# Kernel optimization log

Hardware: AMD Instinct MI355X
Metric: run time of the kernel (lower is better)

The kernel has to match this reference:

```python
import jax, jax.numpy as jnp
from jax import lax
import numpy as np


def setup_inputs() -> dict:
    key = jax.random.key(0)
    kx, kw = jax.random.split(key)
    # Binary {0,1} activations: the module's int8-cast/XOR/AND trick is only
    # meaningful XNOR-popcount math for binary inputs.
    x = jax.random.randint(kx, (32, 256, 58, 58), 0, 2).astype(jnp.float32)
    weight = jax.random.normal(kw, (256, 256, 3, 3), dtype=jnp.float32)
    return {"x": x, "weight": weight}


def reference(x, weight):
    # XNORConv2d.forward, stride=1, padding=0 (forward never pads).
    B, C, H, W = x.shape
    O, _, kh, kw = weight.shape
    n = C * H * W  # note: alpha normalizes by INPUT size, as in the source
    N = kh * kw

    # alpha = sum_{c,kh,kw} |w| / n, one scalar per output filter  -> (O,)
    alpha = jnp.sum(jnp.abs(weight), axis=(1, 2, 3)) / n

    # Binarized weights: sign(w) >= 0 -> {0,1}
    bw = (weight >= 0).astype(x.dtype)

    dn = lax.conv_dimension_numbers(x.shape, weight.shape, ("NCHW", "OIHW", "NCHW"))
    conv = lambda a, f: lax.conv_general_dilated(
        a, f, window_strides=(1, 1), padding="VALID", dimension_numbers=dn
    )

    # XNOR match count per (b, o, y, x): S = #(p==f) over c,kh,kw
    #   = conv(p, f) + conv(1-p, 1-f)
    S = conv(x, bw) + conv(1.0 - x, 1.0 - bw)  # (B, O, H', W')

    # popcount per channel = 2*s_c - N; summed over channels -> 2*S - C*N
    res = 2.0 * S - jnp.asarray(C * N, dtype=x.dtype)

    return alpha[None, :, None, None] * res
```

## Files before the change

kernel.cpp:

```cpp
#include <hip/hip_runtime.h>
#include <stdint.h>


#define BATCH 32
#define C_IN 256
#define OCH 256
#define HIN 58
#define WIN2 58
#define HOUT 56
#define WOUT 56
#define TAPS 9
#define WWORDS 8
#define HWIN (HIN * WIN2)
#define HWOUT (HOUT * WOUT)
#define NPOS (BATCH * HWIN)
#define OGRP 32

__global__ __launch_bounds__(256) void pack_x_kernel(
    const float* __restrict__ x, uint32_t* __restrict__ xp)
{
    int t = blockIdx.x * 256 + threadIdx.x;
    int w = t / (NPOS / 2);
    int q = t - w * (NPOS / 2);
    int p = 2 * q;
    int b = p / HWIN;
    int r = p - b * HWIN;
    const float* xb = x + ((size_t)(b * C_IN + w * 32)) * HWIN + r;
    uint32_t m0 = 0u, m1 = 0u;
    #pragma unroll
    for (int j = 0; j < 32; ++j) {
        float2 v = *(const float2*)(xb + (size_t)j * HWIN);
        m0 |= (v.x > 0.5f ? 1u : 0u) << j;
        m1 |= (v.y > 0.5f ? 1u : 0u) << j;
    }
    xp[(size_t)p * WWORDS + w] = m0;
    xp[(size_t)(p + 1) * WWORDS + w] = m1;
}

__global__ __launch_bounds__(256) void pack_w_kernel(
    const float* __restrict__ wt, uint32_t* __restrict__ wq,
    float* __restrict__ sA, float* __restrict__ sB)
{
    int o = blockIdx.x;
    int c = threadIdx.x;
    const float* wb = wt + ((size_t)o * C_IN + c) * TAPS;
    float wv[TAPS];
    float s = 0.f;
    #pragma unroll
    for (int t = 0; t < TAPS; ++t) {
        wv[t] = wb[t];
        s += fabsf(wv[t]);
    }
    int wave = c >> 6, lane = c & 63;
    #pragma unroll
    for (int t = 0; t < TAPS; ++t) {
        unsigned long long m = __ballot(wv[t] >= 0.0f);
        if (lane == 0) {
            wq[((size_t)t * OCH + o) * WWORDS + wave * 2]     = (uint32_t)m;
            wq[((size_t)t * OCH + o) * WWORDS + wave * 2 + 1] = (uint32_t)(m >> 32);
        }
    }
    __shared__ float red[256];
    red[c] = s;
    __syncthreads();
    for (int off = 128; off > 0; off >>= 1) {
        if (c < off) red[c] += red[c + off];
        __syncthreads();
    }
    if (c == 0) {
        float alpha = red[0] / (float)(C_IN * HWIN);
        sA[o] = -2.0f * alpha;
        sB[o] = (float)(C_IN * TAPS) * alpha;
    }
}

__global__ __launch_bounds__(256, 4) void xnor_main_kernel(
    const uint32_t* __restrict__ xp, const uint32_t* __restrict__ wq,
    const float* __restrict__ sA, const float* __restrict__ sB,
    float* __restrict__ out)
{
    __shared__ uint32_t wlds[TAPS * OGRP * WWORDS];

    int obase = blockIdx.y * OGRP;
    #pragma unroll
    for (int i = 0; i < 9; ++i) {
        int L = threadIdx.x + i * 256;
        int tap = L >> 8;
        int oo  = (L >> 3) & (OGRP - 1);
        int k   = L & 7;
        wlds[L] = wq[(((size_t)tap * OCH) + obase + oo) * WWORDS + k];
    }
    __syncthreads();

    int m = blockIdx.x * 256 + threadIdx.x;
    int b = m / HWOUT;
    int r = m - b * HWOUT;
    int oy = r / WOUT;
    int ox = r - oy * WOUT;

    uint32_t acc[OGRP / 2];
    #pragma unroll
    for (int i = 0; i < OGRP / 2; ++i) acc[i] = 0u;

    #pragma unroll 1
    for (int tap = 0; tap < TAPS; ++tap) {
        int dy = tap / 3, dx = tap - dy * 3;
        const uint4* src = (const uint4*)(xp +
            (((size_t)b * HIN + (oy + dy)) * WIN2 + (ox + dx)) * WWORDS);
        uint4 x0 = src[0];
        uint4 x1 = src[1];
        const uint4* wl = (const uint4*)&wlds[tap * OGRP * WWORDS];
        #pragma unroll
        for (int oo = 0; oo < OGRP; oo += 2) {
            uint4 wa = wl[oo * 2 + 0];
            uint4 wb2 = wl[oo * 2 + 1];
            uint4 wc = wl[oo * 2 + 2];
            uint4 wd = wl[oo * 2 + 3];
            uint32_t q0 = __popc(wa.x ^ x0.x) + __popc(wa.y ^ x0.y)
                        + __popc(wa.z ^ x0.z) + __popc(wa.w ^ x0.w);
            uint32_t q1 = __popc(wb2.x ^ x1.x) + __popc(wb2.y ^ x1.y)
                        + __popc(wb2.z ^ x1.z) + __popc(wb2.w ^ x1.w);
            uint32_t q2 = __popc(wc.x ^ x0.x) + __popc(wc.y ^ x0.y)
                        + __popc(wc.z ^ x0.z) + __popc(wc.w ^ x0.w);
            uint32_t q3 = __popc(wd.x ^ x1.x) + __popc(wd.y ^ x1.y)
                        + __popc(wd.z ^ x1.z) + __popc(wd.w ^ x1.w);
            acc[oo >> 1] += (q0 + q1) + ((q2 + q3) << 16);
        }
    }

    size_t ob = ((size_t)b * OCH + obase) * HWOUT + (size_t)oy * WOUT + ox;
    #pragma unroll
    for (int oo = 0; oo < OGRP; oo += 2) {
        uint32_t a = acc[oo >> 1];
        float P0 = (float)(a & 0xFFFFu);
        float P1 = (float)(a >> 16);
        int o0 = obase + oo;
        out[ob + (size_t)oo * HWOUT]       = fmaf(sA[o0],     P0, sB[o0]);
        out[ob + (size_t)(oo + 1) * HWOUT] = fmaf(sA[o0 + 1], P1, sB[o0 + 1]);
    }
}

extern "C" void kernel_launch(void* const* d_in, const int* in_sizes, int n_in,
                              void* d_out, int out_size, void* d_ws, size_t ws_size,
                              hipStream_t stream)
{
    const float* x  = (const float*)d_in[0];
    const float* wt = (const float*)d_in[1];
    float* out = (float*)d_out;

    char* ws = (char*)d_ws;
    uint32_t* xp = (uint32_t*)ws;
    uint32_t* wq = (uint32_t*)(ws + 3444736);
    float*    sA = (float*)(ws + 3444736 + 73728);
    float*    sB = (float*)(ws + 3444736 + 73728 + 1024);

    pack_x_kernel<<<dim3(1682), dim3(256), 0, stream>>>(x, xp);

    pack_w_kernel<<<dim3(OCH), dim3(256), 0, stream>>>(wt, wq, sA, sB);

    xnor_main_kernel<<<dim3(392, 8), dim3(256), 0, stream>>>(xp, wq, sA, sB, out);
}
```

Measured before the change: 316.8 us.

## Prefetch next tap's packed input, restructure packing writes, raise occupancy target

The main XNOR kernel now loads the next tap's packed activation words while computing the current tap, which hides global load latency behind popcount work. It also raises the launch-bounds occupancy hint from 4 to 8 blocks per CU, which limits registers per thread. The popcount accumulation is reordered so popcounts feed the accumulator directly, a form that may map onto the bitcount-accumulate instruction. The x packing kernel now has each thread handle one position and two 32-channel words, writing one 8-byte store instead of two strided 4-byte stores. In exchange the packing reads become scalar and less coalesced per lane, and the higher occupancy target risks register spilling.

```diff
diff --git a/kernel.cpp b/kernel.cpp
--- a/kernel.cpp
+++ b/kernel.cpp
@@ -20,21 +20,20 @@
     const float* __restrict__ x, uint32_t* __restrict__ xp)
 {
     int t = blockIdx.x * 256 + threadIdx.x;
-    int w = t / (NPOS / 2);
-    int q = t - w * (NPOS / 2);
-    int p = 2 * q;
+    int p  = t >> 2;
+    int wp = t & 3;
     int b = p / HWIN;
     int r = p - b * HWIN;
-    const float* xb = x + ((size_t)(b * C_IN + w * 32)) * HWIN + r;
+    const float* xb = x + ((size_t)(b * C_IN + wp * 64)) * HWIN + r;
     uint32_t m0 = 0u, m1 = 0u;
     #pragma unroll
     for (int j = 0; j < 32; ++j) {
-        float2 v = *(const float2*)(xb + (size_t)j * HWIN);
-        m0 |= (v.x > 0.5f ? 1u : 0u) << j;
-        m1 |= (v.y > 0.5f ? 1u : 0u) << j;
+        float v0 = xb[(size_t)j * HWIN];
+        float v1 = xb[(size_t)(j + 32) * HWIN];
+        m0 |= (v0 > 0.5f ? 1u : 0u) << j;
+        m1 |= (v1 > 0.5f ? 1u : 0u) << j;
     }
-    xp[(size_t)p * WWORDS + w] = m0;
-    xp[(size_t)(p + 1) * WWORDS + w] = m1;
+    *(uint2*)(xp + (size_t)p * WWORDS + wp * 2) = make_uint2(m0, m1);
 }
 
 __global__ __launch_bounds__(256) void pack_w_kernel(
@@ -74,12 +73,12 @@
     }
 }
 
-__global__ __launch_bounds__(256, 4) void xnor_main_kernel(
+__global__ __launch_bounds__(256, 8) void xnor_main_kernel(
     const uint32_t* __restrict__ xp, const uint32_t* __restrict__ wq,
     const float* __restrict__ sA, const float* __restrict__ sB,
     float* __restrict__ out)
 {
-    __shared__ uint32_t wlds[TAPS * OGRP * WWORDS];
+    __shared__ __attribute__((aligned(16))) uint32_t wlds[TAPS * OGRP * WWORDS];
 
     int obase = blockIdx.y * OGRP;
     #pragma unroll
@@ -98,34 +97,43 @@
     int oy = r / WOUT;
     int ox = r - oy * WOUT;
 
+    const uint32_t* xrow = xp + (((size_t)b * HIN + oy) * WIN2 + ox) * WWORDS;
+
     uint32_t acc[OGRP / 2];
     #pragma unroll
     for (int i = 0; i < OGRP / 2; ++i) acc[i] = 0u;
 
+    uint4 x0 = *(const uint4*)(xrow);
+    uint4 x1 = *(const uint4*)(xrow + 4);
+
     #pragma unroll 1
     for (int tap = 0; tap < TAPS; ++tap) {
-        int dy = tap / 3, dx = tap - dy * 3;
-        const uint4* src = (const uint4*)(xp +
-            (((size_t)b * HIN + (oy + dy)) * WIN2 + (ox + dx)) * WWORDS);
-        uint4 x0 = src[0];
-        uint4 x1 = src[1];
-        const uint4* wl = (const uint4*)&wlds[tap * OGRP * WWORDS];
+        int t2 = (tap < TAPS - 1) ? tap + 1 : TAPS - 1;
+        int dy2 = t2 / 3;
+        int dx2 = t2 - dy2 * 3;
+        const uint32_t* nsrc = xrow + (size_t)(dy2 * WIN2 + dx2) * WWORDS;
+        uint4 nx0 = *(const uint4*)(nsrc);
+        uint4 nx1 = *(const uint4*)(nsrc + 4);
+
+        const uint4* wl = (const uint4*)(wlds + tap * OGRP * WWORDS);
         #pragma unroll
         for (int oo = 0; oo < OGRP; oo += 2) {
-            uint4 wa = wl[oo * 2 + 0];
+            uint4 wa  = wl[oo * 2 + 0];
             uint4 wb2 = wl[oo * 2 + 1];
-            uint4 wc = wl[oo * 2 + 2];
-            uint4 wd = wl[oo * 2 + 3];
-            uint32_t q0 = __popc(wa.x ^ x0.x) + __popc(wa.y ^ x0.y)
-                        + __popc(wa.z ^ x0.z) + __popc(wa.w ^ x0.w);
-            uint32_t q1 = __popc(wb2.x ^ x1.x) + __popc(wb2.y ^ x1.y)
-                        + __popc(wb2.z ^ x1.z) + __popc(wb2.w ^ x1.w);
-            uint32_t q2 = __popc(wc.x ^ x0.x) + __popc(wc.y ^ x0.y)
-                        + __popc(wc.z ^ x0.z) + __popc(wc.w ^ x0.w);
-            uint32_t q3 = __popc(wd.x ^ x1.x) + __popc(wd.y ^ x1.y)
+            uint4 wc  = wl[oo * 2 + 2];
+            uint4 wd  = wl[oo * 2 + 3];
+            uint32_t a = acc[oo >> 1];
+            a += __popc(wa.x ^ x0.x); a += __popc(wa.y ^ x0.y);
+            a += __popc(wa.z ^ x0.z); a += __popc(wa.w ^ x0.w);
+            a += __popc(wb2.x ^ x1.x); a += __popc(wb2.y ^ x1.y);
+            a += __popc(wb2.z ^ x1.z); a += __popc(wb2.w ^ x1.w);
+            uint32_t qo = __popc(wc.x ^ x0.x) + __popc(wc.y ^ x0.y)
+                        + __popc(wc.z ^ x0.z) + __popc(wc.w ^ x0.w)
+                        + __popc(wd.x ^ x1.x) + __popc(wd.y ^ x1.y)
                         + __popc(wd.z ^ x1.z) + __popc(wd.w ^ x1.w);
-            acc[oo >> 1] += (q0 + q1) + ((q2 + q3) << 16);
+            acc[oo >> 1] = a + (qo << 16);
         }
+        x0 = nx0; x1 = nx1;
     }
 
     size_t ob = ((size_t)b * OCH + obase) * HWOUT + (size_t)oy * WOUT + ox;
```

New measurement: 319.4 us. About the same (+0.8%).
